# Kernel optimization log

Hardware: AMD Instinct MI355X
Metric: run time of the kernel (lower is better)

Reference implementation:

```python
import jax, jax.numpy as jnp
import numpy as np
import math

N = 2_000_000
NUM_LEVELS = 16
MIN_RES, MAX_RES = 16, 2048
FEAT = 2
GROWTH = math.exp((math.log(MAX_RES) - math.log(MIN_RES)) / (NUM_LEVELS - 1))
RES = np.array([int(MIN_RES * GROWTH ** i) for i in range(NUM_LEVELS)], dtype=np.int32)
# Source bug (replicated faithfully): hash is taken mod len(hash_tables[0].weight) = min(16**3, 2**19) = 4096 for ALL levels.
HASH_MOD = min(MIN_RES ** 3, 2 ** 19)  # 4096
PRIMES_MOD = np.array([1 % HASH_MOD, 2654435761 % HASH_MOD, 805459861 % HASH_MOD], dtype=np.int32)
HID, GEO, HIDC, APP = 64, 15, 64, 32


def _lin(key, fin, fout):
    k1, k2 = jax.random.split(key)
    return (jax.random.normal(k1, (fin, fout), jnp.float32) * 0.05,
            jax.random.normal(k2, (fout,), jnp.float32) * 0.01)


def setup_inputs() -> dict:
    key = jax.random.key(0)
    ks = jax.random.split(key, 16)
    inp = {}
    inp['ray_samples'] = jax.random.normal(ks[0], (N, 3), jnp.float32)
    inp['directions'] = jax.random.normal(ks[1], (N, 3), jnp.float32)
    inp['camera_indices'] = jax.random.randint(ks[2], (N,), 0, 1000, jnp.int32)
    inp['aabb'] = jnp.array([[-1.0, -1.0, -1.0], [1.0, 1.0, 1.0]], jnp.float32)
    # hash tables: only first HASH_MOD rows are reachable (source mod bug); init uniform(-1e-4, 1e-4)
    inp['hash_tables'] = jax.random.uniform(ks[3], (NUM_LEVELS, HASH_MOD, FEAT), jnp.float32, -1e-4, 1e-4)
    inp['dir_w1'], inp['dir_b1'] = _lin(ks[4], 3, 16)
    inp['dir_w2'], inp['dir_b2'] = _lin(ks[5], 16, 16)
    inp['dens_w1'], inp['dens_b1'] = _lin(ks[6], NUM_LEVELS * FEAT, HID)
    inp['dens_w2'], inp['dens_b2'] = _lin(ks[7], HID, HID)
    inp['dens_w3'], inp['dens_b3'] = _lin(ks[8], HID, 1 + GEO)
    cin = GEO + 16 + APP  # 63
    inp['col_w1'], inp['col_b1'] = _lin(ks[9], cin, HIDC)
    inp['col_w2'], inp['col_b2'] = _lin(ks[10], HIDC, HIDC)
    inp['col_w3'], inp['col_b3'] = _lin(ks[11], HIDC, 3)
    inp['app_emb'] = jax.random.normal(ks[12], (1000, APP), jnp.float32) * 0.01
    return inp


def hash_encode(positions, hash_tables):
    # positions: [N,3] in [0,1]; hash_tables: [L, HASH_MOD, FEAT]
    res = jnp.asarray(RES)  # [L]
    scaled = positions[None, :, :] * (res[:, None, None] - 1).astype(jnp.float32)  # [L,N,3]
    coords = jnp.clip(jnp.floor(scaled).astype(jnp.int32), 0, res[:, None, None] - 1)
    # (coords * primes).sum(-1) % HASH_MOD, computed mod-safe in int32
    h = (coords * jnp.asarray(PRIMES_MOD)).sum(-1) % HASH_MOD  # [L,N]
    feats = hash_tables[jnp.arange(NUM_LEVELS)[:, None], h]  # [L,N,FEAT] (no trilinear interp, per source)
    return jnp.transpose(feats, (1, 0, 2)).reshape(positions.shape[0], NUM_LEVELS * FEAT)  # [N,32]


def reference(ray_samples, directions, camera_indices, aabb, hash_tables,
              dir_w1, dir_b1, dir_w2, dir_b2,
              dens_w1, dens_b1, dens_w2, dens_b2, dens_w3, dens_b3,
              col_w1, col_b1, col_w2, col_b2, col_w3, col_b3, app_emb):
    positions = jnp.clip((ray_samples - aabb[0]) / (aabb[1] - aabb[0]), 0.0, 1.0)
    enc = hash_encode(positions, hash_tables)  # [N,32]
    h = jax.nn.relu(enc @ dens_w1 + dens_b1)
    h = jax.nn.relu(h @ dens_w2 + dens_b2)
    dfeat = h @ dens_w3 + dens_b3  # [N,16]
    density = jax.nn.relu(dfeat[:, :1])
    geo = dfeat[:, 1:]
    edir = jax.nn.relu(directions @ dir_w1 + dir_b1) @ dir_w2 + dir_b2  # [N,16]
    cin = jnp.concatenate([geo, edir, app_emb[camera_indices]], axis=-1)  # [N,63]
    c = jax.nn.relu(cin @ col_w1 + col_b1)
    c = jax.nn.relu(c @ col_w2 + col_b2)
    rgb = jax.nn.sigmoid(c @ col_w3 + col_b3)  # [N,3]
    return jnp.concatenate([rgb, density, geo], axis=-1)  # [N,19]
```

## Files before the change

### kernel.cpp

```cpp
#include <hip/hip_runtime.h>
#include <math.h>


typedef short short8 __attribute__((ext_vector_type(8)));
typedef float f32x4 __attribute__((ext_vector_type(4)));
typedef float f32x4a __attribute__((ext_vector_type(4), aligned(4)));
typedef float f32x2a __attribute__((ext_vector_type(2), aligned(4)));
typedef unsigned int uint;
typedef unsigned short ushort;

struct EncC { float rf[16]; };

#define PY 2481
#define PZ 1941

#define MFMA(A,B,C) __builtin_amdgcn_mfma_f32_16x16x32_bf16(A, B, C, 0, 0, 0)

#define W1_OFF   0
#define W3_OFF   5120
#define C3_OFF   7424
#define DB1_OFF  9728
#define DB2_OFF  9984
#define DB3_OFF  10240
#define CB1_OFF  10304
#define CB2_OFF  10560
#define CB3_OFF  10816
#define W2_OFF   10848
#define C1_OFF   20064
#define C2_OFF   29280
#define ACT_OFF  10848
#define LDS_BYTES 47712

__device__ __forceinline__ uint bf16rne(float x) {
    uint u = __builtin_bit_cast(uint, x);
    return (u + 0x7fffu + ((u >> 16) & 1u)) >> 16;
}
__device__ __forceinline__ uint pktr(float lo, float hi) {
    return __builtin_amdgcn_perm(__builtin_bit_cast(uint, hi),
                                 __builtin_bit_cast(uint, lo), 0x07060302u);
}

__device__ __forceinline__ void layer_wb(const f32x4* acc, char* rowp, int q) {
#pragma unroll
    for (int mt = 0; mt < 4; ++mt) {
        const f32x4 v = acc[mt];
        uint2 pw;
        pw.x = pktr(fmaxf(v[0], 0.f), fmaxf(v[1], 0.f));
        pw.y = pktr(fmaxf(v[2], 0.f), fmaxf(v[3], 0.f));
        *(uint2*)(rowp + mt*32 + q*8) = pw;
    }
}

__device__ __forceinline__ void layer64(char* wact, const short8* aw,
                                        const char* biasp, int l15, int q) {
    const int q16 = q * 16;
    f32x4 bf[4];
#pragma unroll
    for (int mt = 0; mt < 4; ++mt)
        bf[mt] = *(const f32x4*)(biasp + mt*64 + q16);
#pragma unroll
    for (int nt = 0; nt < 4; ++nt) {
        char* rowp = wact + (nt*16 + l15)*144;
        short8 b0 = *(const short8*)(rowp + q16);
        short8 b1 = *(const short8*)(rowp + 64 + q16);
        f32x4 acc[4];
#pragma unroll
        for (int mt = 0; mt < 4; ++mt) {
            f32x4 z = MFMA(aw[2*mt], b0, bf[mt]);
            acc[mt] = MFMA(aw[2*mt + 1], b1, z);
        }
        layer_wb(acc, rowp, q);
    }
}

__global__ __launch_bounds__(256, 3)
void nerf_mfma(const float* __restrict__ ray, const float* __restrict__ dirs,
               const int* __restrict__ cam_idx, const float* __restrict__ aabb,
               const float* __restrict__ ht,
               const float* __restrict__ dir_w1, const float* __restrict__ dir_b1,
               const float* __restrict__ dir_w2, const float* __restrict__ dir_b2,
               const float* __restrict__ dens_w1, const float* __restrict__ dens_b1,
               const float* __restrict__ dens_w2, const float* __restrict__ dens_b2,
               const float* __restrict__ dens_w3, const float* __restrict__ dens_b3,
               const float* __restrict__ col_w1, const float* __restrict__ col_b1,
               const float* __restrict__ col_w2, const float* __restrict__ col_b2,
               const float* __restrict__ col_w3, const float* __restrict__ col_b3,
               const float* __restrict__ app_emb,
               float* __restrict__ out, int n, EncC enc)
{
    __shared__ __align__(16) char smem[LDS_BYTES];
    const int t = threadIdx.x;

    {
        uint* z = (uint*)smem;
        for (int i = t; i < 38496/4; i += 256) z[i] = 0;
    }
    __syncthreads();
    {
        ushort* w1t = (ushort*)(smem + W1_OFF);
        for (int e = t; e < 2048; e += 256) w1t[(e&63)*40 + (e>>6)] = (ushort)bf16rne(dens_w1[e]);
        ushort* w2t = (ushort*)(smem + W2_OFF);
        for (int e = t; e < 4096; e += 256) w2t[(e&63)*72 + (e>>6)] = (ushort)bf16rne(dens_w2[e]);
        ushort* w3t = (ushort*)(smem + W3_OFF);
        for (int e = t; e < 1024; e += 256) w3t[(e&15)*72 + (e>>4)] = (ushort)bf16rne(dens_w3[e]);
        ushort* c1t = (ushort*)(smem + C1_OFF);
        for (int e = t; e < 4032; e += 256) {
            int in = e >> 6, o = e & 63;
            int pk = (in < 15) ? (in + 49) : ((in < 31) ? (in + 17) : (in - 31));
            c1t[o*72 + pk] = (ushort)bf16rne(col_w1[e]);
        }
        ushort* c2t = (ushort*)(smem + C2_OFF);
        for (int e = t; e < 4096; e += 256) c2t[(e&63)*72 + (e>>6)] = (ushort)bf16rne(col_w2[e]);
        ushort* c3t = (ushort*)(smem + C3_OFF);
        for (int e = t; e < 192; e += 256) c3t[(e%3)*72 + (e/3)] = (ushort)bf16rne(col_w3[e]);
        if (t < 64) {
            *(float*)(smem + DB1_OFF + t*4) = dens_b1[t];
            *(float*)(smem + DB2_OFF + t*4) = dens_b2[t];
            *(float*)(smem + CB1_OFF + t*4) = col_b1[t];
            *(float*)(smem + CB2_OFF + t*4) = col_b2[t];
        }
        if (t < 16) *(float*)(smem + DB3_OFF + t*4) = dens_b3[t];
        if (t < 4)  *(float*)(smem + CB3_OFF + t*4) = (t < 3) ? col_b3[t] : 0.f;
    }
    __syncthreads();

    const int w = t >> 6, lane = t & 63, l15 = lane & 15, q = lane >> 4;
    const int q16 = q * 16;
    char* wact = smem + ACT_OFF + w*9216;

    short8 aD2[8], aC1[8], aC2[8];
#pragma unroll
    for (int mt = 0; mt < 4; ++mt)
#pragma unroll
        for (int kk = 0; kk < 2; ++kk) {
            const int ro = (mt*16 + l15)*144 + kk*64 + q16;
            aD2[mt*2+kk] = *(const short8*)(smem + W2_OFF + ro);
            aC1[mt*2+kk] = *(const short8*)(smem + C1_OFF + ro);
            aC2[mt*2+kk] = *(const short8*)(smem + C2_OFF + ro);
        }
    __syncthreads();

    const float a0x = aabb[0], a0y = aabb[1], a0z = aabb[2];
    const float ivx = 1.f/(aabb[3]-a0x), ivy = 1.f/(aabb[4]-a0y), ivz = 1.f/(aabb[5]-a0z);

    const int ntiles = (n + 255) >> 8;
    for (int tile = blockIdx.x; tile < ntiles; tile += gridDim.x) {
        const int base = tile*256 + w*64;
        if (base >= n) continue;
        const bool full = (base + 64 <= n);
        const int sc = full ? (base + lane) : min(base + lane, n - 1);
        float* otile = out + (size_t)base * 19;

        float px = fminf(fmaxf((ray[3*sc  ] - a0x)*ivx, 0.f), 1.f);
        float py = fminf(fmaxf((ray[3*sc+1] - a0y)*ivy, 0.f), 1.f);
        float pz = fminf(fmaxf((ray[3*sc+2] - a0z)*ivz, 0.f), 1.f);
        uint encp[16];
#pragma unroll
        for (int l = 0; l < 16; ++l) {
            const float rf = enc.rf[l];
            const int cx = (int)(px*rf), cy = (int)(py*rf), cz = (int)(pz*rf);
            const int h = (cx + cy*PY + cz*PZ) & 4095;
            const float2 f = *(const float2*)(ht + (((l<<12) + h) << 1));
            encp[l] = pktr(f.x, f.y);
        }
        uint4* arow = (uint4*)(wact + lane*144);
        arow[0] = make_uint4(encp[0],  encp[1],  encp[2],  encp[3]);
        arow[1] = make_uint4(encp[4],  encp[5],  encp[6],  encp[7]);
        arow[2] = make_uint4(encp[8],  encp[9],  encp[10], encp[11]);
        arow[3] = make_uint4(encp[12], encp[13], encp[14], encp[15]);

        {
            short8 a1[4];
            f32x4 bf[4];
#pragma unroll
            for (int mt = 0; mt < 4; ++mt) {
                a1[mt] = *(const short8*)(smem + W1_OFF + (mt*16 + l15)*80 + q16);
                bf[mt] = *(const f32x4*)(smem + DB1_OFF + mt*64 + q16);
            }
#pragma unroll
            for (int nt = 0; nt < 4; ++nt) {
                char* rowp = wact + (nt*16 + l15)*144;
                short8 b = *(const short8*)(rowp + q16);
                f32x4 acc[4];
#pragma unroll
                for (int mt = 0; mt < 4; ++mt)
                    acc[mt] = MFMA(a1[mt], b, bf[mt]);
                layer_wb(acc, rowp, q);
            }
        }
        layer64(wact, aD2, smem + DB2_OFF, l15, q);
        {
            short8 a0 = *(const short8*)(smem + W3_OFF + l15*144 + q16);
            short8 a1 = *(const short8*)(smem + W3_OFF + l15*144 + 64 + q16);
            f32x4 bb3 = *(const f32x4*)(smem + DB3_OFF + q16);
#pragma unroll
            for (int nt = 0; nt < 4; ++nt) {
                char* rowp = wact + (nt*16 + l15)*144;
                short8 b0 = *(const short8*)(rowp + q16);
                short8 b1 = *(const short8*)(rowp + 64 + q16);
                f32x4 z = MFMA(a0, b0, bb3);
                f32x4 v = MFMA(a1, b1, z);
                uint2 g;
                g.x = pktr(q == 0 ? 0.f : v[0], v[1]);
                g.y = pktr(v[2], v[3]);
                *(uint2*)(rowp + 96 + 8*q) = g;
                if (q == 0) v[0] = fmaxf(v[0], 0.f);
                const int sg = nt*16 + l15;
                if (full || base + sg < n)
                    *(f32x4a*)(otile + sg*19 + 3 + q16/4) = v;
            }
        }
        {
            const float dx = dirs[3*sc], dy = dirs[3*sc+1], dz = dirs[3*sc+2];
            float e1[16];
#pragma unroll
            for (int j = 0; j < 16; ++j)
                e1[j] = fmaxf(fmaf(dx, dir_w1[j],
                              fmaf(dy, dir_w1[16+j],
                              fmaf(dz, dir_w1[32+j], dir_b1[j]))), 0.f);
            float ed[16];
#pragma unroll
            for (int j = 0; j < 16; ++j) ed[j] = dir_b2[j];
#pragma unroll
            for (int i = 0; i < 16; ++i) {
                const float e = e1[i];
#pragma unroll
                for (int j = 0; j < 16; ++j) ed[j] = fmaf(e, dir_w2[i*16+j], ed[j]);
            }
            const int cam = cam_idx[sc];
            const float4* ap = (const float4*)(app_emb + (size_t)cam*32);
            uint pk[16];
#pragma unroll
            for (int qd = 0; qd < 8; ++qd) {
                const float4 vv = ap[qd];
                pk[2*qd]   = pktr(vv.x, vv.y);
                pk[2*qd+1] = pktr(vv.z, vv.w);
            }
            arow[0] = make_uint4(pk[0],  pk[1],  pk[2],  pk[3]);
            arow[1] = make_uint4(pk[4],  pk[5],  pk[6],  pk[7]);
            arow[2] = make_uint4(pk[8],  pk[9],  pk[10], pk[11]);
            arow[3] = make_uint4(pk[12], pk[13], pk[14], pk[15]);
            uint ep[8];
#pragma unroll
            for (int j = 0; j < 8; ++j) ep[j] = pktr(ed[2*j], ed[2*j+1]);
            arow[4] = make_uint4(ep[0], ep[1], ep[2], ep[3]);
            arow[5] = make_uint4(ep[4], ep[5], ep[6], ep[7]);
        }
        layer64(wact, aC1, smem + CB1_OFF, l15, q);
        layer64(wact, aC2, smem + CB2_OFF, l15, q);
        {
            short8 a0 = *(const short8*)(smem + C3_OFF + l15*144 + q16);
            short8 a1 = *(const short8*)(smem + C3_OFF + l15*144 + 64 + q16);
            f32x4 bbc = *(const f32x4*)(smem + CB3_OFF);
#pragma unroll
            for (int nt = 0; nt < 4; ++nt) {
                char* rowp = wact + (nt*16 + l15)*144;
                short8 b0 = *(const short8*)(rowp + q16);
                short8 b1 = *(const short8*)(rowp + 64 + q16);
                f32x4 z = MFMA(a0, b0, bbc);
                f32x4 v = MFMA(a1, b1, z);
                const int sg = nt*16 + l15;
                if (q == 0 && (full || base + sg < n)) {
                    float* op = otile + sg*19;
                    f32x2a r01;
                    r01[0] = 1.f / (1.f + __expf(-v[0]));
                    r01[1] = 1.f / (1.f + __expf(-v[1]));
                    *(f32x2a*)op = r01;
                    op[2] = 1.f / (1.f + __expf(-v[2]));
                }
            }
        }
    }
}

extern "C" void kernel_launch(void* const* d_in, const int* in_sizes, int n_in,
                              void* d_out, int out_size, void* d_ws, size_t ws_size,
                              hipStream_t stream)
{
    const float* ray  = (const float*)d_in[0];
    const float* dirs = (const float*)d_in[1];
    const int*   cam  = (const int*)  d_in[2];
    const float* aabb = (const float*)d_in[3];
    const float* ht   = (const float*)d_in[4];
    const float* dw1  = (const float*)d_in[5];
    const float* db1  = (const float*)d_in[6];
    const float* dw2  = (const float*)d_in[7];
    const float* db2  = (const float*)d_in[8];
    const float* nw1  = (const float*)d_in[9];
    const float* nb1  = (const float*)d_in[10];
    const float* nw2  = (const float*)d_in[11];
    const float* nb2  = (const float*)d_in[12];
    const float* nw3  = (const float*)d_in[13];
    const float* nb3  = (const float*)d_in[14];
    const float* cw1  = (const float*)d_in[15];
    const float* cb1  = (const float*)d_in[16];
    const float* cw2  = (const float*)d_in[17];
    const float* cb2  = (const float*)d_in[18];
    const float* cw3  = (const float*)d_in[19];
    const float* cb3  = (const float*)d_in[20];
    const float* app  = (const float*)d_in[21];
    float* out = (float*)d_out;

    const int n = in_sizes[0] / 3;

    EncC enc;
    const double growth = exp((log(2048.0) - log(16.0)) / 15.0);
    for (int i = 0; i < 16; ++i) {
        const int r = (int)(16.0 * pow(growth, (double)i));
        enc.rf[i] = (float)(r - 1);
    }

    const int ntiles = (n + 255) / 256;
    const int grid = ntiles < 768 ? ntiles : 768;
    nerf_mfma<<<grid, 256, 0, stream>>>(
        ray, dirs, cam, aabb, ht,
        dw1, db1, dw2, db2,
        nw1, nb1, nw2, nb2, nw3, nb3,
        cw1, cb1, cw2, cb2, cw3, cb3,
        app, out, n, enc);
}
```

Measured before the change: 418.3 us.

## Software-pipeline input loads and hash encoding across grid-stride tiles

Input loads for the next tile (ray, direction, camera index) are issued at the start of the current tile. Hash-grid encoding and the direction MLP for the next tile run at the end of the current iteration and are carried in registers, so global-memory latency can overlap with the MFMA layers. This adds about 25 live registers per lane, which risks spills or lower occupancy under the 3-blocks-per-SM launch bound, and it adds a redundant prefetch past the last tile. The output offset expression was also rewritten from q16/4 to 4*q, which is equivalent.

```diff
diff --git a/kernel.cpp b/kernel.cpp
--- a/kernel.cpp
+++ b/kernel.cpp
@@ -71,6 +71,44 @@
         }
         layer_wb(acc, rowp, q);
     }
+}
+
+__device__ __forceinline__ void stage_inputs(
+    float rx, float ry, float rz, float dx, float dy, float dz,
+    float a0x, float a0y, float a0z, float ivx, float ivy, float ivz,
+    const float* __restrict__ ht,
+    const float* __restrict__ dir_w1, const float* __restrict__ dir_b1,
+    const float* __restrict__ dir_w2, const float* __restrict__ dir_b2,
+    const EncC& enc, uint* encp, uint* ep)
+{
+    const float px = fminf(fmaxf((rx - a0x)*ivx, 0.f), 1.f);
+    const float py = fminf(fmaxf((ry - a0y)*ivy, 0.f), 1.f);
+    const float pz = fminf(fmaxf((rz - a0z)*ivz, 0.f), 1.f);
+#pragma unroll
+    for (int l = 0; l < 16; ++l) {
+        const float rf = enc.rf[l];
+        const int cx = (int)(px*rf), cy = (int)(py*rf), cz = (int)(pz*rf);
+        const int h = (cx + cy*PY + cz*PZ) & 4095;
+        const float2 f = *(const float2*)(ht + (((l<<12) + h) << 1));
+        encp[l] = pktr(f.x, f.y);
+    }
+    float e1[16];
+#pragma unroll
+    for (int j = 0; j < 16; ++j)
+        e1[j] = fmaxf(fmaf(dx, dir_w1[j],
+                      fmaf(dy, dir_w1[16+j],
+                      fmaf(dz, dir_w1[32+j], dir_b1[j]))), 0.f);
+    float ed[16];
+#pragma unroll
+    for (int j = 0; j < 16; ++j) ed[j] = dir_b2[j];
+#pragma unroll
+    for (int i = 0; i < 16; ++i) {
+        const float e = e1[i];
+#pragma unroll
+        for (int j = 0; j < 16; ++j) ed[j] = fmaf(e, dir_w2[i*16+j], ed[j]);
+    }
+#pragma unroll
+    for (int j = 0; j < 8; ++j) ep[j] = pktr(ed[2*j], ed[2*j+1]);
 }
 
 __global__ __launch_bounds__(256, 3)
@@ -144,30 +182,35 @@
     const float ivx = 1.f/(aabb[3]-a0x), ivy = 1.f/(aabb[4]-a0y), ivz = 1.f/(aabb[5]-a0z);
 
     const int ntiles = (n + 255) >> 8;
-    for (int tile = blockIdx.x; tile < ntiles; tile += gridDim.x) {
+    const int stride = gridDim.x;
+
+    uint encp_s[16], ep_s[8];
+    int cam_s;
+    {
+        const int sc0 = min(blockIdx.x*256 + w*64 + lane, n - 1);
+        const float rx = ray[3*sc0], ry = ray[3*sc0+1], rz = ray[3*sc0+2];
+        const float dx = dirs[3*sc0], dy = dirs[3*sc0+1], dz = dirs[3*sc0+2];
+        cam_s = cam_idx[sc0];
+        stage_inputs(rx, ry, rz, dx, dy, dz, a0x, a0y, a0z, ivx, ivy, ivz,
+                     ht, dir_w1, dir_b1, dir_w2, dir_b2, enc, encp_s, ep_s);
+    }
+
+    for (int tile = blockIdx.x; tile < ntiles; tile += stride) {
         const int base = tile*256 + w*64;
         if (base >= n) continue;
         const bool full = (base + 64 <= n);
-        const int sc = full ? (base + lane) : min(base + lane, n - 1);
         float* otile = out + (size_t)base * 19;
 
-        float px = fminf(fmaxf((ray[3*sc  ] - a0x)*ivx, 0.f), 1.f);
-        float py = fminf(fmaxf((ray[3*sc+1] - a0y)*ivy, 0.f), 1.f);
-        float pz = fminf(fmaxf((ray[3*sc+2] - a0z)*ivz, 0.f), 1.f);
-        uint encp[16];
-#pragma unroll
-        for (int l = 0; l < 16; ++l) {
-            const float rf = enc.rf[l];
-            const int cx = (int)(px*rf), cy = (int)(py*rf), cz = (int)(pz*rf);
-            const int h = (cx + cy*PY + cz*PZ) & 4095;
-            const float2 f = *(const float2*)(ht + (((l<<12) + h) << 1));
-            encp[l] = pktr(f.x, f.y);
-        }
         uint4* arow = (uint4*)(wact + lane*144);
-        arow[0] = make_uint4(encp[0],  encp[1],  encp[2],  encp[3]);
-        arow[1] = make_uint4(encp[4],  encp[5],  encp[6],  encp[7]);
-        arow[2] = make_uint4(encp[8],  encp[9],  encp[10], encp[11]);
-        arow[3] = make_uint4(encp[12], encp[13], encp[14], encp[15]);
+        arow[0] = make_uint4(encp_s[0],  encp_s[1],  encp_s[2],  encp_s[3]);
+        arow[1] = make_uint4(encp_s[4],  encp_s[5],  encp_s[6],  encp_s[7]);
+        arow[2] = make_uint4(encp_s[8],  encp_s[9],  encp_s[10], encp_s[11]);
+        arow[3] = make_uint4(encp_s[12], encp_s[13], encp_s[14], encp_s[15]);
+
+        const int scn = min((tile + stride)*256 + w*64 + lane, n - 1);
+        const float rxn = ray[3*scn], ryn = ray[3*scn+1], rzn = ray[3*scn+2];
+        const float dxn = dirs[3*scn], dyn = dirs[3*scn+1], dzn = dirs[3*scn+2];
+        const int camn = cam_idx[scn];
 
         {
             short8 a1[4];
@@ -207,28 +250,12 @@
                 if (q == 0) v[0] = fmaxf(v[0], 0.f);
                 const int sg = nt*16 + l15;
                 if (full || base + sg < n)
-                    *(f32x4a*)(otile + sg*19 + 3 + q16/4) = v;
-            }
-        }
+                    *(f32x4a*)(otile + sg*19 + 3 + 4*q) = v;
+            }
+        }
+
         {
-            const float dx = dirs[3*sc], dy = dirs[3*sc+1], dz = dirs[3*sc+2];
-            float e1[16];
-#pragma unroll
-            for (int j = 0; j < 16; ++j)
-                e1[j] = fmaxf(fmaf(dx, dir_w1[j],
-                              fmaf(dy, dir_w1[16+j],
-                              fmaf(dz, dir_w1[32+j], dir_b1[j]))), 0.f);
-            float ed[16];
-#pragma unroll
-            for (int j = 0; j < 16; ++j) ed[j] = dir_b2[j];
-#pragma unroll
-            for (int i = 0; i < 16; ++i) {
-                const float e = e1[i];
-#pragma unroll
-                for (int j = 0; j < 16; ++j) ed[j] = fmaf(e, dir_w2[i*16+j], ed[j]);
-            }
-            const int cam = cam_idx[sc];
-            const float4* ap = (const float4*)(app_emb + (size_t)cam*32);
+            const float4* ap = (const float4*)(app_emb + (size_t)cam_s * 32);
             uint pk[16];
 #pragma unroll
             for (int qd = 0; qd < 8; ++qd) {
@@ -240,12 +267,10 @@
             arow[1] = make_uint4(pk[4],  pk[5],  pk[6],  pk[7]);
             arow[2] = make_uint4(pk[8],  pk[9],  pk[10], pk[11]);
             arow[3] = make_uint4(pk[12], pk[13], pk[14], pk[15]);
-            uint ep[8];
-#pragma unroll
-            for (int j = 0; j < 8; ++j) ep[j] = pktr(ed[2*j], ed[2*j+1]);
-            arow[4] = make_uint4(ep[0], ep[1], ep[2], ep[3]);
-            arow[5] = make_uint4(ep[4], ep[5], ep[6], ep[7]);
-        }
+            arow[4] = make_uint4(ep_s[0], ep_s[1], ep_s[2], ep_s[3]);
+            arow[5] = make_uint4(ep_s[4], ep_s[5], ep_s[6], ep_s[7]);
+        }
+
         layer64(wact, aC1, smem + CB1_OFF, l15, q);
         layer64(wact, aC2, smem + CB2_OFF, l15, q);
         {
@@ -270,6 +295,11 @@
                 }
             }
         }
+
+        cam_s = camn;
+        stage_inputs(rxn, ryn, rzn, dxn, dyn, dzn, a0x, a0y, a0z,
+                     ivx, ivy, ivz, ht, dir_w1, dir_b1, dir_w2, dir_b2,
+                     enc, encp_s, ep_s);
     }
 }
 
```

Result: slower. 441.2 us (+5.5%).
